# Performance work log

Measured on AMD Instinct MI355X. Metric: run time of the kernel, lower is better.

Reference implementation:

```python
import jax, jax.numpy as jnp
import numpy as np

B, S, DIN, DIM, H = 2, 2304, 1024, 1024, 16
HEAD_DIM = DIM // H            # 64
ROT_DIM = HEAD_DIM             # partial_rotary_factor = 1
BASE = 10000.0
EPS = 1e-6


def setup_inputs() -> dict:
    key = jax.random.key(0)
    ks = jax.random.split(key, 6)
    return {
        "input": jax.random.normal(ks[0], (B, S, DIN), dtype=jnp.float32),
        "qkv_w": jax.random.normal(ks[1], (3 * DIM, DIN), dtype=jnp.float32) * 0.02,
        "qkv_b": jnp.zeros((3 * DIM,), dtype=jnp.float32),
        "q_scale": jnp.ones((DIM,), dtype=jnp.float32),
        "k_scale": jnp.ones((DIM,), dtype=jnp.float32),
        "proj_w": jax.random.normal(ks[2], (DIN, DIM), dtype=jnp.float32) * 0.02,
        "proj_b": jnp.zeros((DIN,), dtype=jnp.float32),
        "height": 48,
        "width": 48,
    }


def _rms_norm(x, scale):
    # RMSNorm over the full inner dim (QKNorm), learned scale
    var = jnp.mean(x * x, axis=-1, keepdims=True)
    return x * jax.lax.rsqrt(var + EPS) * scale


def _rope_1d(x, pos):
    # x: (b, n, h, d_ax), pos: (n,) float; rotate_half-style RoPE
    d = x.shape[-1]
    inv_freq = 1.0 / (BASE ** (jnp.arange(0, d, 2, dtype=jnp.float32) / d))  # (d/2,)
    ang = pos[:, None] * inv_freq                                            # (n, d/2)
    cos = jnp.concatenate([jnp.cos(ang), jnp.cos(ang)], axis=-1)[None, :, None, :]
    sin = jnp.concatenate([jnp.sin(ang), jnp.sin(ang)], axis=-1)[None, :, None, :]
    x1, x2 = jnp.split(x, 2, axis=-1)
    rot = jnp.concatenate([-x2, x1], axis=-1)
    return x * cos + rot * sin


def _rope_2d(x, height, width):
    # axial 2D RoPE: first half of rotary dims keyed by row, second half by col
    n = height * width
    idx = jnp.arange(n, dtype=jnp.float32)
    rows = jnp.floor(idx / width)
    cols = jnp.mod(idx, width)
    half = ROT_DIM // 2
    x_r = _rope_1d(x[..., :half], rows)
    x_c = _rope_1d(x[..., half:ROT_DIM], cols)
    return jnp.concatenate([x_r, x_c, x[..., ROT_DIM:]], axis=-1)


def reference(input, qkv_w, qkv_b, q_scale, k_scale, proj_w, proj_b, height, width):
    b, n, _ = input.shape
    qkv = input @ qkv_w.T + qkv_b                       # (b, n, 3*dim)
    q, k, v = jnp.split(qkv, 3, axis=-1)
    q = _rms_norm(q, q_scale)
    k = _rms_norm(k, k_scale)
    # (b, n, h, d)
    q = q.reshape(b, n, H, HEAD_DIM)
    k = k.reshape(b, n, H, HEAD_DIM)
    v = v.reshape(b, n, H, HEAD_DIM)
    q = _rope_2d(q, height, width)
    k = _rope_2d(k, height, width)
    scale = HEAD_DIM ** (-0.5)
    # (b, h, q, k)
    scores = jnp.einsum("bqhd,bkhd->bhqk", q, k) * scale
    attn = jax.nn.softmax(scores, axis=-1)
    out = jnp.einsum("bhqk,bkhd->bqhd", attn, v)        # (b, n, h, d)
    out = out.reshape(b, n, DIM)
    return out @ proj_w.T + proj_b
```

## Files before the change

kernel.cpp:

```cpp
#include <hip/hip_runtime.h>
#include <math.h>

#define BB   2
#define SS   2304
#define DINC 1024
#define DIMC 1024
#define HH   16
#define HD   64

typedef _Float16 half_t;
typedef __attribute__((ext_vector_type(4))) _Float16 half4;
typedef __attribute__((ext_vector_type(8))) _Float16 half8;
typedef __attribute__((ext_vector_type(4))) float    f32x4;

#define LOG2E 1.44269504088896340736f
#define EXP2(x) __builtin_amdgcn_exp2f(x)

#define GLOAD_LDS16(gp, lp)                                                     \
    __builtin_amdgcn_global_load_lds(                                           \
        (const __attribute__((address_space(1))) void*)(gp),                    \
        (__attribute__((address_space(3))) void*)(lp), 16, 0, 0)

template<int RB>
__device__ __forceinline__
void conv_body(const float* __restrict__ src, half_t* __restrict__ dst,
               int K, int mb, int kb, int t)
{
    constexpr int NG = RB * 32 / 1024;
    const float* sp0 = src + (size_t)mb * RB * K + kb * 32;
    half_t*      dp0 = dst + ((size_t)mb * (K >> 5) + kb) * (RB * 32);
    #pragma unroll
    for (int g = 0; g < NG; ++g) {
        const int e  = g * 1024 + t * 4;
        const int mm = e >> 5, kk = e & 31;
        float4 v = *(const float4*)(sp0 + (size_t)mm * K + kk);
        dp0[e + 0] = (half_t)v.x; dp0[e + 1] = (half_t)v.y;
        dp0[e + 2] = (half_t)v.z; dp0[e + 3] = (half_t)v.w;
    }
}

__global__ __launch_bounds__(256)
void convert_all_f16(const float* __restrict__ input, const float* __restrict__ qkv_w,
                     const float* __restrict__ proj_w, half_t* __restrict__ Ah,
                     half_t* __restrict__ Bh1, half_t* __restrict__ Bh2)
{
    const int bx = blockIdx.x;
    const int kb = blockIdx.y;
    const int t  = threadIdx.x;
    if (bx < 24)      conv_body<192>(input, Ah,  DINC, bx,      kb, t);
    else if (bx < 56) conv_body<96>(qkv_w, Bh1, DINC, bx - 24, kb, t);
    else              conv_body<64>(proj_w, Bh2, DIMC, bx - 56, kb, t);
}

__global__ __launch_bounds__(256, 3)
void gemm_mfma192(const half_t* __restrict__ Ah, const half_t* __restrict__ Bh,
                  const float* __restrict__ bias, half_t* __restrict__ Cout)
{
    const int t    = threadIdx.x;
    const int w    = t >> 6;
    const int lane = t & 63;
    const int l15  = lane & 15, quad = lane >> 4;
    const int wr   = w >> 1;
    const int wc   = w & 1;
    const int mb   = blockIdx.y;
    const int nb   = blockIdx.x;

    __shared__ __align__(16) half_t smem[18432];

    f32x4 acc[6][3];
    #pragma unroll
    for (int mt = 0; mt < 6; ++mt)
        #pragma unroll
        for (int nt = 0; nt < 3; ++nt) acc[mt][nt] = (f32x4){0.f, 0.f, 0.f, 0.f};

    const half_t* atile = Ah + (size_t)mb * 32 * 6144;
    const half_t* btile = Bh + (size_t)nb * 32 * 3072;

    #define STAGE192(s, bsel)                                                   \
    {                                                                           \
        const half_t* at = atile + (size_t)(s) * 6144;                          \
        const half_t* bt = btile + (size_t)(s) * 3072;                          \
        half_t* dstA = smem + (bsel) * 9216;                                    \
        half_t* dstB = dstA + 6144;                                             \
        for (int ch = w; ch < 18; ch += 4) {                                    \
            if (ch < 12) GLOAD_LDS16(at + ch * 512 + lane * 8, dstA + ch * 512);\
            else         GLOAD_LDS16(bt + (ch - 12) * 512 + lane * 8,           \
                                     dstB + (ch - 12) * 512);                   \
        }                                                                       \
    }

    STAGE192(0, 0);
    __syncthreads();

    for (int s = 0; s < 32; ++s) {
        const int b = s & 1;
        if (s + 1 < 32) STAGE192(s + 1, b ^ 1);

        const half_t* Au = smem + b * 9216;
        const half_t* Bu = Au + 6144;
        half8 af[6], bf[3];
        #pragma unroll
        for (int mt = 0; mt < 6; ++mt)
            af[mt] = *(const half8*)(Au + (wr * 96 + mt * 16 + l15) * 32 + quad * 8);
        #pragma unroll
        for (int nt = 0; nt < 3; ++nt)
            bf[nt] = *(const half8*)(Bu + (wc * 48 + nt * 16 + l15) * 32 + quad * 8);
        #pragma unroll
        for (int mt = 0; mt < 6; ++mt)
            #pragma unroll
            for (int nt = 0; nt < 3; ++nt)
                acc[mt][nt] = __builtin_amdgcn_mfma_f32_16x16x32_f16(
                    af[mt], bf[nt], acc[mt][nt], 0, 0, 0);

        __syncthreads();
    }
    #undef STAGE192

    const int bm = mb * 192, bn = nb * 96;
    #pragma unroll
    for (int nt = 0; nt < 3; ++nt) {
        const int lc = wc * 48 + nt * 16 + l15;
        const float bv = bias[bn + lc];
        #pragma unroll
        for (int mt = 0; mt < 6; ++mt) {
            const int lr0 = wr * 96 + mt * 16 + quad * 4;
            #pragma unroll
            for (int rg = 0; rg < 4; ++rg)
                smem[(lr0 + rg) * 96 + lc] = (half_t)(acc[mt][nt][rg] + bv);
        }
    }
    __syncthreads();

    #pragma unroll
    for (int i = 0; i < 9; ++i) {
        const int g   = t + 256 * i;
        const int lr  = g / 12;
        const int lc8 = (g % 12) * 8;
        *(half8*)(Cout + (size_t)(bm + lr) * 3072 + bn + lc8)
            = *(const half8*)(smem + lr * 96 + lc8);
    }
}

template<int BN, bool OUT_HALF>
__global__ __launch_bounds__(256)
void gemm_mfma(const half_t* __restrict__ Ah, const half_t* __restrict__ Bh,
               const float* __restrict__ bias, void* __restrict__ Cout,
               int M, int N, int K)
{
    constexpr int MT = (BN == 128) ? 4 : 2;
    constexpr int NT = 4;
    const int KB = K >> 5;
    __shared__ half_t As[8192];
    __shared__ half_t Bs[2 * BN * 32];

    const int t    = threadIdx.x;
    const int w    = t >> 6;
    const int lane = t & 63;
    const int l15  = lane & 15, quad = lane >> 4;
    const int wr   = (BN == 128) ? (w >> 1) : w;
    const int wc   = (BN == 128) ? (w & 1) : 0;
    const int mb   = blockIdx.y, nb = blockIdx.x;

    f32x4 acc[MT][NT];
    #pragma unroll
    for (int mt = 0; mt < MT; ++mt)
        #pragma unroll
        for (int nt = 0; nt < NT; ++nt) acc[mt][nt] = (f32x4){0.f, 0.f, 0.f, 0.f};

    const half_t* atile = Ah + (size_t)mb * KB * 4096;
    const half_t* btile = Bh + (size_t)nb * KB * (BN * 32);

    for (int kb = 0; kb < KB; kb += 2) {
        #pragma unroll
        for (int u = 0; u < 2; ++u) {
            const half_t* at = atile + (size_t)(kb + u) * 4096;
            const half_t* bt = btile + (size_t)(kb + u) * (BN * 32);
            #pragma unroll
            for (int v = 0; v < 2; ++v) {
                const int ch = w * 2 + v;
                GLOAD_LDS16(at + ch * 512 + lane * 8, As + u * 4096 + ch * 512);
            }
            GLOAD_LDS16(bt + w * 512 + lane * 8, Bs + u * (BN * 32) + w * 512);
        }
        __syncthreads();

        #pragma unroll
        for (int u = 0; u < 2; ++u) {
            half8 af[MT], bf[NT];
            #pragma unroll
            for (int mt = 0; mt < MT; ++mt)
                af[mt] = *(const half8*)(As + u * 4096
                                         + (wr * (MT * 16) + mt * 16 + l15) * 32 + quad * 8);
            #pragma unroll
            for (int nt = 0; nt < NT; ++nt)
                bf[nt] = *(const half8*)(Bs + u * (BN * 32)
                                         + (wc * 64 + nt * 16 + l15) * 32 + quad * 8);
            #pragma unroll
            for (int mt = 0; mt < MT; ++mt)
                #pragma unroll
                for (int nt = 0; nt < NT; ++nt)
                    acc[mt][nt] = __builtin_amdgcn_mfma_f32_16x16x32_f16(
                        af[mt], bf[nt], acc[mt][nt], 0, 0, 0);
        }
        __syncthreads();
    }

    const int bm = mb * 128, bn = nb * BN;
    #pragma unroll
    for (int nt = 0; nt < NT; ++nt) {
        const int n  = bn + wc * 64 + nt * 16 + l15;
        const float bv = bias[n];
        #pragma unroll
        for (int mt = 0; mt < MT; ++mt) {
            const int m0 = bm + wr * (MT * 16) + mt * 16 + quad * 4;
            #pragma unroll
            for (int rg = 0; rg < 4; ++rg) {
                const float v = acc[mt][nt][rg] + bv;
                if (OUT_HALF) ((half_t*)Cout)[(size_t)(m0 + rg) * N + n] = (half_t)v;
                else          ((float*) Cout)[(size_t)(m0 + rg) * N + n] = v;
            }
        }
    }
}

__global__ __launch_bounds__(256)
void normrope_v8(half_t* __restrict__ qkvh, const float* __restrict__ q_scale,
                 const float* __restrict__ k_scale, const int* __restrict__ wptr,
                 half_t* __restrict__ Kf, half_t* __restrict__ Vf)
{
    const int token = blockIdx.x;
    const int s     = token % SS;
    const int b     = token / SS;
    const int w     = *wptr;
    const int t     = threadIdx.x;
    const float rowp = (float)(s / w);
    const float colp = (float)(s % w);

    half_t* base = qkvh + (size_t)token * 3072;

    const int c    = s >> 5;
    const int slot = s & 31;
    const int ktile = (slot >> 2) & 1;
    const int krow  = ((slot >> 3) << 2) + (slot & 3);

    {
        half4 v4 = *(const half4*)(base + 2048 + 4 * t);
        const int dabs0 = 4 * t;
        const int h  = dabs0 >> 6;
        const int sl3 = slot >> 3, sl7 = slot & 7;
        half_t* vdst = Vf + ((size_t)(b * HH + h) * 72 + c) * 2048;
        #pragma unroll
        for (int ii = 0; ii < 4; ++ii) {
            const int d = (dabs0 + ii) & 63;
            vdst[(d >> 4) * 512 + (sl3 * 16 + (d & 15)) * 8 + sl7] = v4[ii];
        }
    }

    __shared__ float buf[DIMC];
    __shared__ float red[4];
    __shared__ __align__(16) half_t obuf[DIMC];

    #pragma unroll
    for (int sel = 0; sel < 2; ++sel) {
        half_t* row = base + sel * DIMC;
        const float* scp = sel ? k_scale : q_scale;

        half4 xh = *(const half4*)(row + 4 * t);
        float x0 = (float)xh[0], x1 = (float)xh[1], x2 = (float)xh[2], x3 = (float)xh[3];
        float ss = x0 * x0 + x1 * x1 + x2 * x2 + x3 * x3;
        #pragma unroll
        for (int o = 32; o >= 1; o >>= 1) ss += __shfl_xor(ss, o);
        if ((t & 63) == 0) red[t >> 6] = ss;
        __syncthreads();

        const float rinv = rsqrtf((red[0] + red[1] + red[2] + red[3]) * (1.0f / DIMC) + 1e-6f);
        float4 g = *(const float4*)(scp + 4 * t);
        buf[4 * t + 0] = x0 * rinv * g.x;
        buf[4 * t + 1] = x1 * rinv * g.y;
        buf[4 * t + 2] = x2 * rinv * g.z;
        buf[4 * t + 3] = x3 * rinv * g.w;
        __syncthreads();

        const float qsc = sel ? 1.0f : (0.125f * LOG2E);

        #pragma unroll
        for (int pp = 0; pp < 2; ++pp) {
            const int p = t + pp * 256;
            const int h = p >> 5;
            const int r = p & 31;
            const int j = r & 15;
            const float pos = (r < 16) ? rowp : colp;
            const int d1 = (r < 16) ? j : (32 + j);
            const int d2 = d1 + 16;
            const float freq = exp2f((float)j * -0.83048202372f);
            const float ang  = pos * freq;
            float sn, cs;
            __sincosf(ang, &sn, &cs);
            const float a1 = buf[h * HD + d1], a2 = buf[h * HD + d2];
            obuf[h * HD + d1] = (half_t)((a1 * cs - a2 * sn) * qsc);
            obuf[h * HD + d2] = (half_t)((a2 * cs + a1 * sn) * qsc);
        }
        __syncthreads();

        if (t < 128) {
            if (sel == 0) {
                *(half8*)(row + t * 8) = *(const half8*)(obuf + t * 8);
            } else {
                const int h = t >> 3, grp = t & 7;
                half_t* kdst = Kf + ((size_t)(b * HH + h) * 72 + c) * 2048;
                const int off = (((ktile << 1) + (grp >> 2)) << 9)
                              + ((((grp & 3) << 4) + krow) << 3);
                *(half8*)(kdst + off) = *(const half8*)(obuf + h * HD + grp * 8);
            }
        }
        __syncthreads();
    }
}

__global__ __launch_bounds__(256, 3)
void flash_attn_mfma17(const half_t* __restrict__ qkvh, const half_t* __restrict__ Kf,
                       const half_t* __restrict__ Vf, half_t* __restrict__ attn_h)
{
    const int flat = blockIdx.x;
    const int xcd  = flat & 7;
    const int idx  = flat >> 3;
    const int bh   = xcd * 4 + idx / 24;
    const int qtb  = idx % 24;
    const int b    = bh >> 4, h = bh & 15;
    const int t    = threadIdx.x;
    const int w    = t >> 6;
    const int qh   = w >> 1;
    const int jt   = w & 1;
    const int lane = t & 63;
    const int l15  = lane & 15, quad = lane >> 4;

    const size_t tb = (size_t)b * SS;
    const int q0 = qtb * 96;

    __shared__ float mlb[4][48];
    __shared__ float Ob[2][64][49];

    half8 qf[3][2];
    #pragma unroll
    for (int qt = 0; qt < 3; ++qt)
        #pragma unroll
        for (int dg = 0; dg < 2; ++dg)
            qf[qt][dg] = *(const half8*)(qkvh + (tb + q0 + qh * 48 + qt * 16 + l15) * 3072
                                          + h * HD + dg * 32 + quad * 8);

    const half8 onesA = (l15 == 0)
        ? (half8){(half_t)1, (half_t)1, (half_t)1, (half_t)1,
                  (half_t)1, (half_t)1, (half_t)1, (half_t)1}
        : (half8){(half_t)0, (half_t)0, (half_t)0, (half_t)0,
                  (half_t)0, (half_t)0, (half_t)0, (half_t)0};

    f32x4 acc[4][3];
    f32x4 acc5[3];
    #pragma unroll
    for (int qt = 0; qt < 3; ++qt) {
        acc5[qt] = (f32x4){0.f, 0.f, 0.f, 0.f};
        #pragma unroll
        for (int dt = 0; dt < 4; ++dt) acc[dt][qt] = (f32x4){0.f, 0.f, 0.f, 0.f};
    }

    const half_t* kpl = Kf + (size_t)bh * 147456 + jt * 2048 + lane * 8;
    const half_t* vpl = Vf + (size_t)bh * 147456 + jt * 2048 + lane * 8;

    half8 k00 = *(const half8*)(kpl);
    half8 k01 = *(const half8*)(kpl + 512);
    half8 k10 = *(const half8*)(kpl + 1024);
    half8 k11 = *(const half8*)(kpl + 1536);
    half8 v0  = *(const half8*)(vpl);
    half8 v1  = *(const half8*)(vpl + 512);
    half8 v2  = *(const half8*)(vpl + 1024);
    half8 v3  = *(const half8*)(vpl + 1536);

    const f32x4 initC = (f32x4){-4.f, -4.f, -4.f, -4.f};

    for (int p = 0; p < 36; ++p) {
        f32x4 scA[3], scB[3];
        __builtin_amdgcn_s_setprio(1);
        #pragma unroll
        for (int qt = 0; qt < 3; ++qt) {
            scA[qt] = initC;
            scA[qt] = __builtin_amdgcn_mfma_f32_16x16x32_f16(k00, qf[qt][0], scA[qt], 0, 0, 0);
            scA[qt] = __builtin_amdgcn_mfma_f32_16x16x32_f16(k01, qf[qt][1], scA[qt], 0, 0, 0);
            scB[qt] = initC;
            scB[qt] = __builtin_amdgcn_mfma_f32_16x16x32_f16(k10, qf[qt][0], scB[qt], 0, 0, 0);
            scB[qt] = __builtin_amdgcn_mfma_f32_16x16x32_f16(k11, qf[qt][1], scB[qt], 0, 0, 0);
        }
        __builtin_amdgcn_s_setprio(0);

        if (p + 1 < 36) {
            const half_t* kN = kpl + (size_t)(p + 1) * 4096;
            k00 = *(const half8*)(kN);
            k01 = *(const half8*)(kN + 512);
            k10 = *(const half8*)(kN + 1024);
            k11 = *(const half8*)(kN + 1536);
        }

        half8 pf[3];
        #pragma unroll
        for (int qt = 0; qt < 3; ++qt) {
            const float a0 = EXP2(scA[qt][0]);
            const float a1 = EXP2(scA[qt][1]);
            const float a2 = EXP2(scA[qt][2]);
            const float a3 = EXP2(scA[qt][3]);
            const float b0 = EXP2(scB[qt][0]);
            const float b1 = EXP2(scB[qt][1]);
            const float b2 = EXP2(scB[qt][2]);
            const float b3 = EXP2(scB[qt][3]);
            pf[qt] = (half8){(half_t)a0, (half_t)a1, (half_t)a2, (half_t)a3,
                             (half_t)b0, (half_t)b1, (half_t)b2, (half_t)b3};
        }

        __builtin_amdgcn_s_setprio(1);
        #pragma unroll
        for (int dt = 0; dt < 4; ++dt) {
            const half8 vf = (dt == 0) ? v0 : (dt == 1) ? v1 : (dt == 2) ? v2 : v3;
            #pragma unroll
            for (int qt = 0; qt < 3; ++qt)
                acc[dt][qt] = __builtin_amdgcn_mfma_f32_16x16x32_f16(
                    vf, pf[qt], acc[dt][qt], 0, 0, 0);
        }
        #pragma unroll
        for (int qt = 0; qt < 3; ++qt)
            acc5[qt] = __builtin_amdgcn_mfma_f32_16x16x32_f16(
                onesA, pf[qt], acc5[qt], 0, 0, 0);
        __builtin_amdgcn_s_setprio(0);

        if (p + 1 < 36) {
            const half_t* vN = vpl + (size_t)(p + 1) * 4096;
            v0 = *(const half8*)(vN);
            v1 = *(const half8*)(vN + 512);
            v2 = *(const half8*)(vN + 1024);
            v3 = *(const half8*)(vN + 1536);
        }
    }

    #pragma unroll
    for (int qt = 0; qt < 3; ++qt)
        if (quad == 0) mlb[w][qt * 16 + l15] = acc5[qt][0];
    __syncthreads();

    float fac[3];
    #pragma unroll
    for (int qt = 0; qt < 3; ++qt) {
        const int q = qt * 16 + l15;
        fac[qt] = 1.0f / (mlb[qh * 2 + 0][q] + mlb[qh * 2 + 1][q]);
    }

    #pragma unroll
    for (int ph = 0; ph < 2; ++ph) {
        if (jt == ph) {
            #pragma unroll
            for (int dt = 0; dt < 4; ++dt)
                #pragma unroll
                for (int qt = 0; qt < 3; ++qt)
                    #pragma unroll
                    for (int rg = 0; rg < 4; ++rg) {
                        const int d = dt * 16 + quad * 4 + rg;
                        const int q = qt * 16 + l15;
                        const float v = acc[dt][qt][rg] * fac[qt];
                        if (ph == 0) Ob[qh][d][q] = v;
                        else         Ob[qh][d][q] += v;
                    }
        }
        __syncthreads();
    }

    #pragma unroll
    for (int g2 = 0; g2 < 3; ++g2) {
        const int q  = g2 * 32 + (t >> 3);
        const int ds = (t & 7) * 8;
        const int qh2 = (q >= 48) ? 1 : 0;
        const int qq  = q - 48 * qh2;
        const size_t mrow = tb + q0 + q;
        const int mb2 = (int)(mrow >> 7);
        const int mm  = (int)(mrow & 127);
        const int kb2 = (h * HD + ds) >> 5;
        const int kk  = ds & 31;
        half8 o;
        #pragma unroll
        for (int ii = 0; ii < 8; ++ii) o[ii] = (half_t)Ob[qh2][ds + ii][qq];
        *(half8*)(attn_h + ((size_t)mb2 * 32 + kb2) * 4096 + mm * 32 + kk) = o;
    }
}

extern "C" void kernel_launch(void* const* d_in, const int* in_sizes, int n_in,
                              void* d_out, int out_size, void* d_ws, size_t ws_size,
                              hipStream_t stream)
{
    const float* input   = (const float*)d_in[0];
    const float* qkv_w   = (const float*)d_in[1];
    const float* qkv_b   = (const float*)d_in[2];
    const float* q_scale = (const float*)d_in[3];
    const float* k_scale = (const float*)d_in[4];
    const float* proj_w  = (const float*)d_in[5];
    const float* proj_b  = (const float*)d_in[6];
    const int*   width   = (const int*)d_in[8];
    float* out = (float*)d_out;

    half_t* qkvh   = (half_t*)d_ws;
    half_t* attn_h = qkvh   + (size_t)4608 * 3072;
    half_t* Vf     = attn_h + (size_t)4608 * 1024;
    half_t* Ah     = Vf     + (size_t)32 * 72 * 2048;
    half_t* Bh1    = Ah     + (size_t)4608 * 1024;
    half_t* Bh2    = Bh1    + (size_t)3072 * 1024;
    half_t* Kf     = Ah;

    const int M = BB * SS;

    convert_all_f16<<<dim3(72, 32), 256, 0, stream>>>(input, qkv_w, proj_w,
                                                      Ah, Bh1, Bh2);

    gemm_mfma192<<<dim3(3 * DIMC / 96, M / 192), 256, 0, stream>>>(
        Ah, Bh1, qkv_b, qkvh);

    normrope_v8<<<M, 256, 0, stream>>>(qkvh, q_scale, k_scale, width, Kf, Vf);

    flash_attn_mfma17<<<dim3(768), 256, 0, stream>>>(qkvh, Kf, Vf, attn_h);

    gemm_mfma<64, false><<<dim3(DINC / 64, M / 128), 256, 0, stream>>>(
        attn_h, Bh2, proj_b, out, M, DINC, DIMC);
}
```

Before: 224.8 us.

## Replace output projection GEMM with 48x128 tiled double-buffered kernel

The generic 128xBN output-projection GEMM is replaced by a specialized kernel using 48x128 tiles. It issues the next k-step's global-to-LDS loads before computing the current one, so there is one barrier per k-step instead of two per pair of steps. The smaller M tile gives 96x8 blocks instead of 36x16, which fills the CUs more evenly, and it sets launch bounds of 3 blocks per CU. The cost is lower per-wave MFMA reuse (3x2 tiles) and strided A-tile addressing into the pre-blocked layout.

```diff
diff --git a/kernel.cpp b/kernel.cpp
--- a/kernel.cpp
+++ b/kernel.cpp
@@ -141,84 +141,85 @@
     }
 }
 
-template<int BN, bool OUT_HALF>
-__global__ __launch_bounds__(256)
-void gemm_mfma(const half_t* __restrict__ Ah, const half_t* __restrict__ Bh,
-               const float* __restrict__ bias, void* __restrict__ Cout,
-               int M, int N, int K)
-{
-    constexpr int MT = (BN == 128) ? 4 : 2;
-    constexpr int NT = 4;
-    const int KB = K >> 5;
-    __shared__ half_t As[8192];
-    __shared__ half_t Bs[2 * BN * 32];
-
+__global__ __launch_bounds__(256, 3)
+void gemm2_48x128(const half_t* __restrict__ Ah, const half_t* __restrict__ Bh,
+                  const float* __restrict__ bias, float* __restrict__ Cout)
+{
     const int t    = threadIdx.x;
     const int w    = t >> 6;
     const int lane = t & 63;
     const int l15  = lane & 15, quad = lane >> 4;
-    const int wr   = (BN == 128) ? (w >> 1) : w;
-    const int wc   = (BN == 128) ? (w & 1) : 0;
-    const int mb   = blockIdx.y, nb = blockIdx.x;
-
-    f32x4 acc[MT][NT];
-    #pragma unroll
-    for (int mt = 0; mt < MT; ++mt)
-        #pragma unroll
-        for (int nt = 0; nt < NT; ++nt) acc[mt][nt] = (f32x4){0.f, 0.f, 0.f, 0.f};
-
-    const half_t* atile = Ah + (size_t)mb * KB * 4096;
-    const half_t* btile = Bh + (size_t)nb * KB * (BN * 32);
-
-    for (int kb = 0; kb < KB; kb += 2) {
-        #pragma unroll
-        for (int u = 0; u < 2; ++u) {
-            const half_t* at = atile + (size_t)(kb + u) * 4096;
-            const half_t* bt = btile + (size_t)(kb + u) * (BN * 32);
+    const int nb   = blockIdx.x;
+    const int mb   = blockIdx.y;
+
+    __shared__ __align__(16) half_t smem[11264];
+
+    f32x4 acc[3][2];
+    #pragma unroll
+    for (int mt = 0; mt < 3; ++mt)
+        #pragma unroll
+        for (int nt = 0; nt < 2; ++nt) acc[mt][nt] = (f32x4){0.f, 0.f, 0.f, 0.f};
+
+    const half_t* bsrc0 = Bh + (size_t)(2 * nb + 0) * 32 * 2048;
+    const half_t* bsrc1 = Bh + (size_t)(2 * nb + 1) * 32 * 2048;
+
+    #define STAGE2(s, bsel)                                                     \
+    {                                                                           \
+        half_t* dstA = smem + (bsel) * 5632;                                    \
+        half_t* dstB = dstA + 1536;                                             \
+        for (int ch = w; ch < 11; ch += 4) {                                    \
+            if (ch < 3) {                                                       \
+                const int mrow0 = mb * 48 + 16 * ch;                            \
+                const half_t* ap = Ah + (size_t)(mrow0 >> 7) * 131072           \
+                                 + (size_t)(s) * 4096 + (mrow0 & 127) * 32;    \
+                GLOAD_LDS16(ap + lane * 8, dstA + ch * 512);                    \
+            } else {                                                            \
+                const int bc = ch - 3;      \
+                const half_t* bp = (bc < 4 ? bsrc0 : bsrc1)                     \
+                                 + (size_t)(s) * 2048 + (bc & 3) * 512;         \
+                GLOAD_LDS16(bp + lane * 8, dstB + bc * 512);                    \
+            }                                                                   \
+        }                                                                       \
+    }
+
+    STAGE2(0, 0);
+    __syncthreads();
+
+    for (int s = 0; s < 32; ++s) {
+        const int b = s & 1;
+        if (s + 1 < 32) STAGE2(s + 1, b ^ 1);
+
+        const half_t* Au = smem + b * 5632;
+        const half_t* Bu = Au + 1536;
+        half8 af[3], bf[2];
+        #pragma unroll
+        for (int mt = 0; mt < 3; ++mt)
+            af[mt] = *(const half8*)(Au + (mt * 16 + l15) * 32 + quad * 8);
+        #pragma unroll
+        for (int nt = 0; nt < 2; ++nt)
+            bf[nt] = *(const half8*)(Bu + (w * 32 + nt * 16 + l15) * 32 + quad * 8);
+        #pragma unroll
+        for (int mt = 0; mt < 3; ++mt)
             #pragma unroll
-            for (int v = 0; v < 2; ++v) {
-                const int ch = w * 2 + v;
-                GLOAD_LDS16(at + ch * 512 + lane * 8, As + u * 4096 + ch * 512);
-            }
-            GLOAD_LDS16(bt + w * 512 + lane * 8, Bs + u * (BN * 32) + w * 512);
-        }
-        __syncthreads();
-
-        #pragma unroll
-        for (int u = 0; u < 2; ++u) {
-            half8 af[MT], bf[NT];
+            for (int nt = 0; nt < 2; ++nt)
+                acc[mt][nt] = __builtin_amdgcn_mfma_f32_16x16x32_f16(
+                    af[mt], bf[nt], acc[mt][nt], 0, 0, 0);
+
+        __syncthreads();
+    }
+    #undef STAGE2
+
+    const int bm = mb * 48, bn = nb * 128;
+    #pragma unroll
+    for (int nt = 0; nt < 2; ++nt) {
+        const int n  = bn + w * 32 + nt * 16 + l15;
+        const float bv = bias[n];
+        #pragma unroll
+        for (int mt = 0; mt < 3; ++mt) {
+            const int m0 = bm + mt * 16 + quad * 4;
             #pragma unroll
-            for (int mt = 0; mt < MT; ++mt)
-                af[mt] = *(const half8*)(As + u * 4096
-                                         + (wr * (MT * 16) + mt * 16 + l15) * 32 + quad * 8);
-            #pragma unroll
-            for (int nt = 0; nt < NT; ++nt)
-                bf[nt] = *(const half8*)(Bs + u * (BN * 32)
-                                         + (wc * 64 + nt * 16 + l15) * 32 + quad * 8);
-            #pragma unroll
-            for (int mt = 0; mt < MT; ++mt)
-                #pragma unroll
-                for (int nt = 0; nt < NT; ++nt)
-                    acc[mt][nt] = __builtin_amdgcn_mfma_f32_16x16x32_f16(
-                        af[mt], bf[nt], acc[mt][nt], 0, 0, 0);
-        }
-        __syncthreads();
-    }
-
-    const int bm = mb * 128, bn = nb * BN;
-    #pragma unroll
-    for (int nt = 0; nt < NT; ++nt) {
-        const int n  = bn + wc * 64 + nt * 16 + l15;
-        const float bv = bias[n];
-        #pragma unroll
-        for (int mt = 0; mt < MT; ++mt) {
-            const int m0 = bm + wr * (MT * 16) + mt * 16 + quad * 4;
-            #pragma unroll
-            for (int rg = 0; rg < 4; ++rg) {
-                const float v = acc[mt][nt][rg] + bv;
-                if (OUT_HALF) ((half_t*)Cout)[(size_t)(m0 + rg) * N + n] = (half_t)v;
-                else          ((float*) Cout)[(size_t)(m0 + rg) * N + n] = v;
-            }
+            for (int rg = 0; rg < 4; ++rg)
+                Cout[(size_t)(m0 + rg) * 1024 + n] = acc[mt][nt][rg] + bv;
         }
     }
 }
@@ -521,6 +522,6 @@
 
     flash_attn_mfma17<<<dim3(768), 256, 0, stream>>>(qkvh, Kf, Vf, attn_h);
 
-    gemm_mfma<64, false><<<dim3(DINC / 64, M / 128), 256, 0, stream>>>(
-        attn_h, Bh2, proj_b, out, M, DINC, DIMC);
-}
+    gemm2_48x128<<<dim3(DINC / 128, M / 48), 256, 0, stream>>>(
+        attn_h, Bh2, proj_b, out);
+}
```

Result: slower. 232.1 us (+3.2%).
